# Kernel optimization log

Hardware: AMD Instinct MI355X
Metric: run time of the kernel (lower is better)

## Reference

```python
import jax, jax.numpy as jnp
import numpy as np

D_MODEL = 1024
NUM_HEADS = 16
HEAD_DIM = D_MODEL // NUM_HEADS
THETA = 10000.0


def _trunc_normal(key, shape, std):
    # approximate trunc_normal_(a=-3std, b=3std) by clipping
    return jnp.clip(jax.random.normal(key, shape) * std, -3 * std, 3 * std)


def setup_inputs() -> dict:
    key = jax.random.key(0)
    ks = jax.random.split(key, 6)
    B, S = 2, 2048
    x = jax.random.normal(ks[0], (B, S, D_MODEL), dtype=jnp.float32)
    token_positions = jnp.sort(
        jax.random.randint(ks[1], (B, S), 0, 2048), axis=-1
    ).astype(jnp.int64)
    std = float(np.sqrt(2.0 / (D_MODEL + D_MODEL)))
    Wq = _trunc_normal(ks[2], (D_MODEL, D_MODEL), std)
    Wk = _trunc_normal(ks[3], (D_MODEL, D_MODEL), std)
    Wv = _trunc_normal(ks[4], (D_MODEL, D_MODEL), std)
    Wo = _trunc_normal(ks[5], (D_MODEL, D_MODEL), std)
    return {"x": x, "Wq": Wq, "Wk": Wk, "Wv": Wv, "Wo": Wo,
            "token_positions": token_positions}


def _rope(x, positions):
    # x: (b, h, s, d), positions: (b, s)
    d = x.shape[-1]
    inv_freq = THETA ** (-jnp.arange(0, d, 2, dtype=jnp.float32) / d)  # (d/2,)
    angles = positions.astype(jnp.float32)[:, None, :, None] * inv_freq  # (b,1,s,d/2)
    cos, sin = jnp.cos(angles), jnp.sin(angles)
    x_even, x_odd = x[..., 0::2], x[..., 1::2]
    out_even = x_even * cos - x_odd * sin
    out_odd = x_even * sin + x_odd * cos
    # interleave back: (..., d/2, 2) -> (..., d)
    return jnp.stack([out_even, out_odd], axis=-1).reshape(x.shape)


def reference(x, Wq, Wk, Wv, Wo, token_positions):
    B, S, _ = x.shape
    H, Dh = NUM_HEADS, HEAD_DIM
    # projections: einsum '... i, o i -> ... o'
    q = jnp.einsum('bsi,oi->bso', x, Wq).reshape(B, S, H, Dh).transpose(0, 2, 1, 3)
    k = jnp.einsum('bsi,oi->bso', x, Wk).reshape(B, S, H, Dh).transpose(0, 2, 1, 3)
    v = jnp.einsum('bsi,oi->bso', x, Wv).reshape(B, S, H, Dh).transpose(0, 2, 1, 3)
    q = _rope(q, token_positions)
    k = _rope(k, token_positions)
    scores = jnp.einsum('bhqd,bhkd->bhqk', q.astype(jnp.float32),
                        k.astype(jnp.float32)) / jnp.sqrt(
        jnp.asarray(Dh, dtype=jnp.float32))
    causal = jnp.tril(jnp.ones((S, S), dtype=bool))
    scores = jnp.where(causal, scores, -jnp.inf)
    attn = jax.nn.softmax(scores, axis=-1)
    out = jnp.einsum('bhqk,bhkd->bhqd', attn, v.astype(jnp.float32)).astype(x.dtype)
    out = out.transpose(0, 2, 1, 3).reshape(B, S, H * Dh)
    return jnp.einsum('bsi,oi->bso', out, Wo)
```

## Files before the change

### kernel.cpp

```cpp
#include <hip/hip_runtime.h>
#include <hip/hip_bf16.h>

#define DMODEL 1024
#define NHEADS 16
#define HDIM   64
#define BATCH  2
#define SEQ    2048
#define XELEMS ((size_t)BATCH * SEQ * DMODEL)
#define WELEMS ((size_t)DMODEL * DMODEL)

typedef __attribute__((ext_vector_type(8))) __bf16 bf16x8;
typedef __attribute__((ext_vector_type(4))) float  f32x4;
typedef __attribute__((ext_vector_type(4))) unsigned int   u32x4;
typedef __attribute__((ext_vector_type(4))) unsigned short u16x4;
typedef __attribute__((ext_vector_type(8))) unsigned short u16x8;

typedef const __attribute__((address_space(1))) void* gas_t;
typedef __attribute__((address_space(3))) void* las_t;

static __device__ __forceinline__ unsigned short f2bf(float f) {
  return __builtin_bit_cast(unsigned short, __float2bfloat16(f));
}
static __device__ __forceinline__ float bf2f(unsigned short u) {
  return __bfloat162float(__builtin_bit_cast(__hip_bfloat16, u));
}

__global__ __launch_bounds__(64) void probe_kernel(const unsigned int* __restrict__ x,
                                                   const int* __restrict__ pos,
                                                   int* __restrict__ flags) {
  const int lane = threadIdx.x;
  int bad = 0;
#pragma unroll
  for (int i = 0; i < 32; ++i) {
    const unsigned int u = x[lane * 32 + i];
    if (((u >> 23) & 0xFFu) == 0xFFu) bad++;
  }
  int zodd = 0;
#pragma unroll
  for (int i = 0; i < 4; ++i)
    if (pos[lane * 8 + 2 * i + 1] == 0) zodd++;
#pragma unroll
  for (int s = 1; s < 64; s <<= 1) {
    bad  += __shfl_xor(bad, s);
    zodd += __shfl_xor(zodd, s);
  }
  if (lane == 0) {
    flags[0] = (bad < 64) ? 1 : 0;
    flags[1] = (zodd >= 200) ? 1 : 0;
  }
}

__global__ __launch_bounds__(256) void conv_kernel(
    const void* __restrict__ x,
    const void* __restrict__ w0, const void* __restrict__ w1,
    const void* __restrict__ w2, const void* __restrict__ w3,
    unsigned short* __restrict__ dst, const int* __restrict__ flags) {
  const size_t e = ((size_t)blockIdx.x * 256 + threadIdx.x) * 8;
  const void* src;
  size_t off;
  if (e < XELEMS) { src = x; off = e; }
  else {
    const size_t r = e - XELEMS;
    const int wi = (int)(r >> 20);
    src = (wi == 0) ? w0 : (wi == 1) ? w1 : (wi == 2) ? w2 : w3;
    off = r & (WELEMS - 1);
  }
  if (flags[0]) {
    const float* s = (const float*)src + off;
    const f32x4 a = *(const f32x4*)(s);
    const f32x4 b = *(const f32x4*)(s + 4);
    u16x8 o8;
#pragma unroll
    for (int j = 0; j < 4; ++j) o8[j] = f2bf(a[j]);
#pragma unroll
    for (int j = 0; j < 4; ++j) o8[4 + j] = f2bf(b[j]);
    *(u16x8*)(dst + e) = o8;
  } else {
    *(u32x4*)(dst + e) = *(const u32x4*)((const unsigned short*)src + off);
  }
}

__device__ __forceinline__ void gemm_core(const unsigned short* __restrict__ Ag,
                                          const unsigned short* __restrict__ Bg,
                                          unsigned short* As, unsigned short* Bs,
                                          int bm, int bn, f32x4 acc[4][4]) {
  const int tid = threadIdx.x;
  const int lane = tid & 63;
  const int w  = tid >> 6;
  const int wm = w >> 1, wn = w & 1;
  const int c = lane & 15, g = lane >> 4;
  const int r0 = tid >> 2;
  const int s0 = (tid & 3) * 8;

  auto stage = [&](int buf, int k0) {
    unsigned short* ad = As + buf * 4096;
    unsigned short* bd = Bs + buf * 4096;
    __builtin_amdgcn_global_load_lds((gas_t)(Ag + (size_t)(bm + r0) * DMODEL + k0 + s0),
                                     (las_t)(ad + tid * 8), 16, 0, 0);
    __builtin_amdgcn_global_load_lds((gas_t)(Ag + (size_t)(bm + r0 + 64) * DMODEL + k0 + s0),
                                     (las_t)(ad + (tid + 256) * 8), 16, 0, 0);
    __builtin_amdgcn_global_load_lds((gas_t)(Bg + (size_t)(bn + r0) * DMODEL + k0 + s0),
                                     (las_t)(bd + tid * 8), 16, 0, 0);
    __builtin_amdgcn_global_load_lds((gas_t)(Bg + (size_t)(bn + r0 + 64) * DMODEL + k0 + s0),
                                     (las_t)(bd + (tid + 256) * 8), 16, 0, 0);
  };

  stage(0, 0);
  __syncthreads();
  for (int k0 = 0; k0 < DMODEL; k0 += 32) {
    const int cur = (k0 >> 5) & 1;
    if (k0 + 32 < DMODEL) stage(cur ^ 1, k0 + 32);
    const unsigned short* ar = As + cur * 4096;
    const unsigned short* br = Bs + cur * 4096;
    bf16x8 af[4], bfr[4];
#pragma unroll
    for (int m = 0; m < 4; ++m)
      af[m] = *(const bf16x8*)&ar[(wm * 64 + m * 16 + c) * 32 + g * 8];
#pragma unroll
    for (int n = 0; n < 4; ++n)
      bfr[n] = *(const bf16x8*)&br[(wn * 64 + n * 16 + c) * 32 + g * 8];
#pragma unroll
    for (int m = 0; m < 4; ++m)
#pragma unroll
      for (int n = 0; n < 4; ++n)
        acc[m][n] = __builtin_amdgcn_mfma_f32_16x16x32_bf16(af[m], bfr[n], acc[m][n], 0, 0, 0);
    __syncthreads();
  }
}

__global__ __launch_bounds__(256) void qkv_gemm_kernel(
    const unsigned short* __restrict__ x,
    const unsigned short* __restrict__ Wq, const unsigned short* __restrict__ Wk,
    const unsigned short* __restrict__ Wv,
    unsigned short* __restrict__ qo, unsigned short* __restrict__ ko,
    unsigned short* __restrict__ vto) {
  __shared__ unsigned short As[2 * 128 * 32];
  __shared__ unsigned short Bs[2 * 128 * 32];
  const int z = blockIdx.z;
  const unsigned short* W = (z == 0) ? Wq : (z == 1) ? Wk : Wv;
  const int bm = blockIdx.x * 128, bn = blockIdx.y * 128;
  f32x4 acc[4][4];
#pragma unroll
  for (int m = 0; m < 4; ++m)
#pragma unroll
    for (int n = 0; n < 4; ++n)
#pragma unroll
      for (int j = 0; j < 4; ++j) acc[m][n][j] = 0.f;

  gemm_core(x, W, As, Bs, bm, bn, acc);

  const int tid = threadIdx.x, lane = tid & 63, w = tid >> 6;
  const int wm = w >> 1, wn = w & 1, c = lane & 15, g4 = lane >> 4;
#pragma unroll
  for (int m = 0; m < 4; ++m) {
#pragma unroll
    for (int n = 0; n < 4; ++n) {
      const int col = bn + wn * 64 + n * 16 + c;
      const int h = col >> 6, d = col & 63;
      const int row0 = bm + wm * 64 + m * 16 + g4 * 4;
      if (z == 2) {
        const int b = row0 >> 11, s0 = row0 & (SEQ - 1);
        u16x4 pk;
#pragma unroll
        for (int j = 0; j < 4; ++j) pk[j] = f2bf(acc[m][n][j]);
        *(u16x4*)&vto[((size_t)(b * NHEADS + h) * HDIM + d) * SEQ + s0] = pk;
      } else {
        unsigned short* dst = z ? ko : qo;
#pragma unroll
        for (int j = 0; j < 4; ++j) {
          const int row = row0 + j;
          const int b = row >> 11, s = row & (SEQ - 1);
          dst[((size_t)(b * NHEADS + h) * SEQ + s) * HDIM + d] = f2bf(acc[m][n][j]);
        }
      }
    }
  }
}

__global__ __launch_bounds__(256) void out_gemm_kernel(
    const unsigned short* __restrict__ A, const unsigned short* __restrict__ Wo,
    void* __restrict__ outv, const int* __restrict__ flags) {
  __shared__ unsigned short As[2 * 128 * 32];
  __shared__ unsigned short Bs[2 * 128 * 32];
  const int bm = blockIdx.x * 128, bn = blockIdx.y * 128;
  f32x4 acc[4][4];
#pragma unroll
  for (int m = 0; m < 4; ++m)
#pragma unroll
    for (int n = 0; n < 4; ++n)
#pragma unroll
      for (int j = 0; j < 4; ++j) acc[m][n][j] = 0.f;

  gemm_core(A, Wo, As, Bs, bm, bn, acc);

  const int tid = threadIdx.x, lane = tid & 63, w = tid >> 6;
  const int wm = w >> 1, wn = w & 1, c = lane & 15, g4 = lane >> 4;
  const int f32o = flags[0];
  if (f32o) {
    float* out = (float*)outv;
#pragma unroll
    for (int m = 0; m < 4; ++m)
#pragma unroll
      for (int n = 0; n < 4; ++n) {
        const int col = bn + wn * 64 + n * 16 + c;
#pragma unroll
        for (int j = 0; j < 4; ++j) {
          const int row = bm + wm * 64 + m * 16 + g4 * 4 + j;
          out[(size_t)row * DMODEL + col] = acc[m][n][j];
        }
      }
  } else {
    unsigned short* out = (unsigned short*)outv;
#pragma unroll
    for (int m = 0; m < 4; ++m)
#pragma unroll
      for (int n = 0; n < 4; ++n) {
        const int col = bn + wn * 64 + n * 16 + c;
#pragma unroll
        for (int j = 0; j < 4; ++j) {
          const int row = bm + wm * 64 + m * 16 + g4 * 4 + j;
          out[(size_t)row * DMODEL + col] = f2bf(acc[m][n][j]);
        }
      }
  }
}

__global__ __launch_bounds__(256) void rope_kernel(unsigned short* __restrict__ q,
                                                   unsigned short* __restrict__ k,
                                                   const int* __restrict__ pos,
                                                   const int* __restrict__ flags) {
  const int idx = blockIdx.x * 256 + threadIdx.x;
  const int tsel = idx >> 21;
  const int p = idx & ((1 << 21) - 1);
  const int j = p & 31;
  const int s = (p >> 5) & (SEQ - 1);
  const int bh = p >> 16;
  const int b = bh >> 4;
  unsigned short* base = tsel ? k : q;
  const int pidx = b * SEQ + s;
  const int pv = flags[1] ? pos[2 * pidx] : pos[pidx];
  const float sc = tsel ? 1.0f : 0.125f;
  const float freq = exp2f((float)j * -0.41524101186092026f);
  const float ang = (float)pv * freq;
  const float cs = cosf(ang);
  const float sn = sinf(ang);
  unsigned int* wp = (unsigned int*)base + ((p >> 5) * 32 + j);
  const unsigned int u = *wp;
  const float e = bf2f((unsigned short)(u & 0xffffu));
  const float o = bf2f((unsigned short)(u >> 16));
  *wp = (unsigned int)f2bf((e * cs - o * sn) * sc) |
        ((unsigned int)f2bf((e * sn + o * cs) * sc) << 16);
}

#define MNEG -1e30f
#define QBLK 64
#define LOG2E 1.4426950408889634f
__global__ __launch_bounds__(256, 3) void flash_kernel(
    const unsigned short* __restrict__ q, const unsigned short* __restrict__ k,
    const unsigned short* __restrict__ vt, unsigned short* __restrict__ o) {
  __shared__ unsigned short Ks[2][64 * 64];
  __shared__ unsigned short Vs[2][64 * 64];
  __shared__ unsigned short Ps[64 * 72];

  const int wg = blockIdx.x;
  const int qt = (SEQ / QBLK - 1) - (wg >> 5);
  const int bh = wg & 31;
  const int qbase = qt * QBLK;
  const int tid = threadIdx.x, lane = tid & 63, w = tid >> 6;
  const int c = lane & 15, g = lane >> 4;
  const int wq = w * 16;
  const size_t tb = (size_t)bh * SEQ * HDIM;

  bf16x8 qf[2];
#pragma unroll
  for (int kk = 0; kk < 2; ++kk)
    qf[kk] = *(const bf16x8*)(q + tb + (size_t)(qbase + wq + c) * HDIM + kk * 32 + g * 8);

  auto stageKV = [&](int buf, int kvb) {
#pragma unroll
    for (int i = 0; i < 2; ++i) {
      const int t = tid + i * 256;
      const int r = t >> 3;
      const int sl = (t & 7) ^ (r & 7);
      __builtin_amdgcn_global_load_lds((gas_t)(k + tb + (size_t)(kvb + r) * HDIM + sl * 8),
                                       (las_t)(Ks[buf] + t * 8), 16, 0, 0);
      __builtin_amdgcn_global_load_lds((gas_t)(vt + tb + (size_t)r * SEQ + kvb + sl * 8),
                                       (las_t)(Vs[buf] + t * 8), 16, 0, 0);
    }
  };

  stageKV(0, 0);
  __syncthreads();

  f32x4 acco[4];
#pragma unroll
  for (int n = 0; n < 4; ++n)
#pragma unroll
    for (int j = 0; j < 4; ++j) acco[n][j] = 0.f;
  float m_r = MNEG, l_r = 0.f;

  const int nkv = qt + 1;
  for (int kt = 0; kt < nkv; ++kt) {
    const int p = kt & 1;
    const int kvb = kt * 64;
    if (kt + 1 < nkv) stageKV(p ^ 1, kvb + 64);

    f32x4 accs[4];
#pragma unroll
    for (int n = 0; n < 4; ++n)
#pragma unroll
      for (int j = 0; j < 4; ++j) accs[n][j] = 0.f;
#pragma unroll
    for (int kk = 0; kk < 2; ++kk)
#pragma unroll
      for (int n = 0; n < 4; ++n) {
        const int r = n * 16 + c;
        const int sl = (kk * 4 + g) ^ (r & 7);
        const bf16x8 ak = *(const bf16x8*)&Ks[p][r * 64 + sl * 8];
        accs[n] = __builtin_amdgcn_mfma_f32_16x16x32_bf16(ak, qf[kk], accs[n], 0, 0, 0);
      }

    const int qg = qbase + wq + c;
    if (kt == qt) {
#pragma unroll
      for (int n = 0; n < 4; ++n)
#pragma unroll
        for (int jj = 0; jj < 4; ++jj)
          if (kvb + n * 16 + g * 4 + jj > qg) accs[n][jj] = MNEG;
    }

    float rm = accs[0][0];
#pragma unroll
    for (int n = 0; n < 4; ++n)
#pragma unroll
      for (int jj = 0; jj < 4; ++jj) rm = fmaxf(rm, accs[n][jj]);
    rm = fmaxf(rm, __shfl_xor(rm, 16));
    rm = fmaxf(rm, __shfl_xor(rm, 32));
    if (!__all(rm <= m_r + 8.f)) {
      const float mn = fmaxf(m_r, rm);
      const float al = exp2f((m_r - mn) * LOG2E);
      l_r *= al;
#pragma unroll
      for (int n = 0; n < 4; ++n)
#pragma unroll
        for (int jj = 0; jj < 4; ++jj) acco[n][jj] *= al;
      m_r = mn;
    }
    float rs = 0.f;
#pragma unroll
    for (int n = 0; n < 4; ++n)
#pragma unroll
      for (int jj = 0; jj < 4; ++jj) {
        const float pv = exp2f((accs[n][jj] - m_r) * LOG2E);
        accs[n][jj] = pv;
        rs += pv;
      }
    rs += __shfl_xor(rs, 16);
    rs += __shfl_xor(rs, 32);
    l_r += rs;

#pragma unroll
    for (int n = 0; n < 4; ++n) {
      u16x4 pk4;
#pragma unroll
      for (int jj = 0; jj < 4; ++jj) pk4[jj] = f2bf(accs[n][jj]);
      *(u16x4*)&Ps[(wq + c) * 72 + n * 16 + g * 4] = pk4;
    }

#pragma unroll
    for (int kk = 0; kk < 2; ++kk) {
      const bf16x8 pb = *(const bf16x8*)&Ps[(wq + c) * 72 + kk * 32 + g * 8];
#pragma unroll
      for (int n = 0; n < 4; ++n) {
        const int r = n * 16 + c;
        const int sl = (kk * 4 + g) ^ (r & 7);
        const bf16x8 av = *(const bf16x8*)&Vs[p][r * 64 + sl * 8];
        acco[n] = __builtin_amdgcn_mfma_f32_16x16x32_bf16(av, pb, acco[n], 0, 0, 0);
      }
    }
    __syncthreads();
  }

  const float rl = 1.f / fmaxf(l_r, 1e-20f);
  const int b = bh >> 4, h = bh & 15;
  const int srow = qbase + wq + c;
#pragma unroll
  for (int n = 0; n < 4; ++n) {
    u16x4 pk;
#pragma unroll
    for (int jj = 0; jj < 4; ++jj) pk[jj] = f2bf(acco[n][jj] * rl);
    *(u16x4*)&o[(size_t)(b * SEQ + srow) * DMODEL + h * 64 + n * 16 + g * 4] = pk;
  }
}

extern "C" void kernel_launch(void* const* d_in, const int* in_sizes, int n_in,
                              void* d_out, int out_size, void* d_ws, size_t ws_size,
                              hipStream_t stream) {
  (void)in_sizes; (void)n_in; (void)out_size; (void)ws_size;
  const size_t MB = (size_t)1 << 20;
  char* ws = (char*)d_ws;
  unsigned short* xb  = (unsigned short*)(ws);
  unsigned short* Wqb = (unsigned short*)(ws + 8 * MB);
  unsigned short* Wkb = (unsigned short*)(ws + 10 * MB);
  unsigned short* Wvb = (unsigned short*)(ws + 12 * MB);
  unsigned short* Wob = (unsigned short*)(ws + 14 * MB);
  unsigned short* qw  = (unsigned short*)(ws + 16 * MB);
  unsigned short* kw  = (unsigned short*)(ws + 24 * MB);
  unsigned short* vtw = (unsigned short*)(ws + 32 * MB);
  int* flags          = (int*)(ws + 40 * MB);
  unsigned short* ow  = xb;

  const dim3 blk(256);
  probe_kernel<<<1, 64, 0, stream>>>((const unsigned int*)d_in[0], (const int*)d_in[5], flags);
  conv_kernel<<<4096, blk, 0, stream>>>(d_in[0], d_in[1], d_in[2], d_in[3], d_in[4], xb, flags);
  qkv_gemm_kernel<<<dim3(32, 8, 3), blk, 0, stream>>>(xb, Wqb, Wkb, Wvb, qw, kw, vtw);
  rope_kernel<<<16384, blk, 0, stream>>>(qw, kw, (const int*)d_in[5], flags);
  flash_kernel<<<dim3(1024), blk, 0, stream>>>(qw, kw, vtw, ow);
  out_gemm_kernel<<<dim3(32, 8), blk, 0, stream>>>(ow, Wob, d_out, flags);
}
```

Baseline: 134.5 us.

## Add MFMA setprio, shrink out-proj tile, unroll flash loop with pointer increments

Wraps the MFMA blocks in s_setprio(1)/(0) in the shared GEMM core and the flash kernel, so waves issuing matrix math get scheduling priority. The output projection moves to a 64x128 tile with its own inline mainloop, doubling the grid from 256 to 512 workgroups for better CU occupancy on the small GEMM. The flash attention loop is unrolled by two with compile-time buffer indices and running K/V pointers, which removes per-iteration address arithmetic. Smaller out-proj tiles lower reuse per workgroup and add more loads of Wo.

```diff
diff --git a/kernel.cpp b/kernel.cpp
--- a/kernel.cpp
+++ b/kernel.cpp
@@ -119,11 +119,13 @@
 #pragma unroll
     for (int n = 0; n < 4; ++n)
       bfr[n] = *(const bf16x8*)&br[(wn * 64 + n * 16 + c) * 32 + g * 8];
+    __builtin_amdgcn_s_setprio(1);
 #pragma unroll
     for (int m = 0; m < 4; ++m)
 #pragma unroll
       for (int n = 0; n < 4; ++n)
         acc[m][n] = __builtin_amdgcn_mfma_f32_16x16x32_bf16(af[m], bfr[n], acc[m][n], 0, 0, 0);
+    __builtin_amdgcn_s_setprio(0);
     __syncthreads();
   }
 }
@@ -180,32 +182,65 @@
 __global__ __launch_bounds__(256) void out_gemm_kernel(
     const unsigned short* __restrict__ A, const unsigned short* __restrict__ Wo,
     void* __restrict__ outv, const int* __restrict__ flags) {
-  __shared__ unsigned short As[2 * 128 * 32];
+  __shared__ unsigned short As[2 * 64 * 32];
   __shared__ unsigned short Bs[2 * 128 * 32];
-  const int bm = blockIdx.x * 128, bn = blockIdx.y * 128;
-  f32x4 acc[4][4];
+  const int bm = blockIdx.x * 64, bn = blockIdx.y * 128;
+  const int tid = threadIdx.x, lane = tid & 63, w = tid >> 6;
+  const int c = lane & 15, g = lane >> 4;
+  const int r0 = tid >> 2, s0 = (tid & 3) * 8;
+  f32x4 acc[4][2];
 #pragma unroll
   for (int m = 0; m < 4; ++m)
 #pragma unroll
-    for (int n = 0; n < 4; ++n)
+    for (int n = 0; n < 2; ++n)
 #pragma unroll
       for (int j = 0; j < 4; ++j) acc[m][n][j] = 0.f;
 
-  gemm_core(A, Wo, As, Bs, bm, bn, acc);
-
-  const int tid = threadIdx.x, lane = tid & 63, w = tid >> 6;
-  const int wm = w >> 1, wn = w & 1, c = lane & 15, g4 = lane >> 4;
+  auto stage = [&](int buf, int k0) {
+    __builtin_amdgcn_global_load_lds((gas_t)(A + (size_t)(bm + r0) * DMODEL + k0 + s0),
+                                     (las_t)(As + buf * 2048 + tid * 8), 16, 0, 0);
+    __builtin_amdgcn_global_load_lds((gas_t)(Wo + (size_t)(bn + r0) * DMODEL + k0 + s0),
+                                     (las_t)(Bs + buf * 4096 + tid * 8), 16, 0, 0);
+    __builtin_amdgcn_global_load_lds((gas_t)(Wo + (size_t)(bn + r0 + 64) * DMODEL + k0 + s0),
+                                     (las_t)(Bs + buf * 4096 + (tid + 256) * 8), 16, 0, 0);
+  };
+
+  stage(0, 0);
+  __syncthreads();
+  for (int k0 = 0; k0 < DMODEL; k0 += 32) {
+    const int cur = (k0 >> 5) & 1;
+    if (k0 + 32 < DMODEL) stage(cur ^ 1, k0 + 32);
+    const unsigned short* ar = As + cur * 2048;
+    const unsigned short* br = Bs + cur * 4096;
+    bf16x8 af[4], bfr[2];
+#pragma unroll
+    for (int m = 0; m < 4; ++m)
+      af[m] = *(const bf16x8*)&ar[(m * 16 + c) * 32 + g * 8];
+#pragma unroll
+    for (int n = 0; n < 2; ++n)
+      bfr[n] = *(const bf16x8*)&br[(w * 32 + n * 16 + c) * 32 + g * 8];
+    __builtin_amdgcn_s_setprio(1);
+#pragma unroll
+    for (int m = 0; m < 4; ++m)
+#pragma unroll
+      for (int n = 0; n < 2; ++n)
+        acc[m][n] = __builtin_amdgcn_mfma_f32_16x16x32_bf16(af[m], bfr[n], acc[m][n], 0, 0, 0);
+    __builtin_amdgcn_s_setprio(0);
+    __syncthreads();
+  }
+
+  const int g4 = g;
   const int f32o = flags[0];
   if (f32o) {
     float* out = (float*)outv;
 #pragma unroll
     for (int m = 0; m < 4; ++m)
 #pragma unroll
-      for (int n = 0; n < 4; ++n) {
-        const int col = bn + wn * 64 + n * 16 + c;
+      for (int n = 0; n < 2; ++n) {
+        const int col = bn + w * 32 + n * 16 + c;
 #pragma unroll
         for (int j = 0; j < 4; ++j) {
-          const int row = bm + wm * 64 + m * 16 + g4 * 4 + j;
+          const int row = bm + m * 16 + g4 * 4 + j;
           out[(size_t)row * DMODEL + col] = acc[m][n][j];
         }
       }
@@ -214,11 +249,11 @@
 #pragma unroll
     for (int m = 0; m < 4; ++m)
 #pragma unroll
-      for (int n = 0; n < 4; ++n) {
-        const int col = bn + wn * 64 + n * 16 + c;
+      for (int n = 0; n < 2; ++n) {
+        const int col = bn + w * 32 + n * 16 + c;
 #pragma unroll
         for (int j = 0; j < 4; ++j) {
-          const int row = bm + wm * 64 + m * 16 + g4 * 4 + j;
+          const int row = bm + m * 16 + g4 * 4 + j;
           out[(size_t)row * DMODEL + col] = f2bf(acc[m][n][j]);
         }
       }
@@ -255,6 +290,106 @@
 #define MNEG -1e30f
 #define QBLK 64
 #define LOG2E 1.4426950408889634f
+
+template<int BUF>
+__device__ __forceinline__ void flash_tile(
+    int kt, int nkv, int qt, int qbase, int wq, int c, int g, int tid,
+    const unsigned short* (&kp)[2], const unsigned short* (&vp)[2],
+    unsigned short (&Ks)[2][64 * 64], unsigned short (&Vs)[2][64 * 64],
+    unsigned short (&Ps)[64 * 72],
+    const bf16x8 (&qf)[2], f32x4 (&acco)[4], float& m_r, float& l_r) {
+  const int kvb = kt * 64;
+  if (kt + 1 < nkv) {
+#pragma unroll
+    for (int i = 0; i < 2; ++i) {
+      const int t8 = (tid + i * 256) * 8;
+      __builtin_amdgcn_global_load_lds((gas_t)kp[i], (las_t)(Ks[BUF ^ 1] + t8), 16, 0, 0);
+      __builtin_amdgcn_global_load_lds((gas_t)vp[i], (las_t)(Vs[BUF ^ 1] + t8), 16, 0, 0);
+      kp[i] += 64 * HDIM;
+      vp[i] += 64;
+    }
+  }
+
+  f32x4 accs[4];
+#pragma unroll
+  for (int n = 0; n < 4; ++n)
+#pragma unroll
+    for (int j = 0; j < 4; ++j) accs[n][j] = 0.f;
+  __builtin_amdgcn_s_setprio(1);
+#pragma unroll
+  for (int kk = 0; kk < 2; ++kk)
+#pragma unroll
+    for (int n = 0; n < 4; ++n) {
+      const int r = n * 16 + c;
+      const int sl = (kk * 4 + g) ^ (r & 7);
+      const bf16x8 ak = *(const bf16x8*)&Ks[BUF][r * 64 + sl * 8];
+      accs[n] = __builtin_amdgcn_mfma_f32_16x16x32_bf16(ak, qf[kk], accs[n], 0, 0, 0);
+    }
+  __builtin_amdgcn_s_setprio(0);
+
+  const int qg = qbase + wq + c;
+  if (kt == qt) {
+#pragma unroll
+    for (int n = 0; n < 4; ++n)
+#pragma unroll
+      for (int jj = 0; jj < 4; ++jj)
+        if (kvb + n * 16 + g * 4 + jj > qg) accs[n][jj] = MNEG;
+  }
+
+  float rm = accs[0][0];
+#pragma unroll
+  for (int n = 0; n < 4; ++n)
+#pragma unroll
+    for (int jj = 0; jj < 4; ++jj) rm = fmaxf(rm, accs[n][jj]);
+  rm = fmaxf(rm, __shfl_xor(rm, 16));
+  rm = fmaxf(rm, __shfl_xor(rm, 32));
+  if (!__all(rm <= m_r + 8.f)) {
+    const float mn = fmaxf(m_r, rm);
+    const float al = exp2f((m_r - mn) * LOG2E);
+    l_r *= al;
+#pragma unroll
+    for (int n = 0; n < 4; ++n)
+#pragma unroll
+      for (int jj = 0; jj < 4; ++jj) acco[n][jj] *= al;
+    m_r = mn;
+  }
+  float rs = 0.f;
+#pragma unroll
+  for (int n = 0; n < 4; ++n)
+#pragma unroll
+    for (int jj = 0; jj < 4; ++jj) {
+      const float pv = exp2f((accs[n][jj] - m_r) * LOG2E);
+      accs[n][jj] = pv;
+      rs += pv;
+    }
+  rs += __shfl_xor(rs, 16);
+  rs += __shfl_xor(rs, 32);
+  l_r += rs;
+
+#pragma unroll
+  for (int n = 0; n < 4; ++n) {
+    u16x4 pk4;
+#pragma unroll
+    for (int jj = 0; jj < 4; ++jj) pk4[jj] = f2bf(accs[n][jj]);
+    *(u16x4*)&Ps[(wq + c) * 72 + n * 16 + g * 4] = pk4;
+  }
+
+  __builtin_amdgcn_s_setprio(1);
+#pragma unroll
+  for (int kk = 0; kk < 2; ++kk) {
+    const bf16x8 pb = *(const bf16x8*)&Ps[(wq + c) * 72 + kk * 32 + g * 8];
+#pragma unroll
+    for (int n = 0; n < 4; ++n) {
+      const int r = n * 16 + c;
+      const int sl = (kk * 4 + g) ^ (r & 7);
+      const bf16x8 av = *(const bf16x8*)&Vs[BUF][r * 64 + sl * 8];
+      acco[n] = __builtin_amdgcn_mfma_f32_16x16x32_bf16(av, pb, acco[n], 0, 0, 0);
+    }
+  }
+  __builtin_amdgcn_s_setprio(0);
+  __syncthreads();
+}
+
 __global__ __launch_bounds__(256, 3) void flash_kernel(
     const unsigned short* __restrict__ q, const unsigned short* __restrict__ k,
     const unsigned short* __restrict__ vt, unsigned short* __restrict__ o) {
@@ -276,20 +411,24 @@
   for (int kk = 0; kk < 2; ++kk)
     qf[kk] = *(const bf16x8*)(q + tb + (size_t)(qbase + wq + c) * HDIM + kk * 32 + g * 8);
 
-  auto stageKV = [&](int buf, int kvb) {
-#pragma unroll
-    for (int i = 0; i < 2; ++i) {
-      const int t = tid + i * 256;
-      const int r = t >> 3;
-      const int sl = (t & 7) ^ (r & 7);
-      __builtin_amdgcn_global_load_lds((gas_t)(k + tb + (size_t)(kvb + r) * HDIM + sl * 8),
-                                       (las_t)(Ks[buf] + t * 8), 16, 0, 0);
-      __builtin_amdgcn_global_load_lds((gas_t)(vt + tb + (size_t)r * SEQ + kvb + sl * 8),
-                                       (las_t)(Vs[buf] + t * 8), 16, 0, 0);
-    }
-  };
-
-  stageKV(0, 0);
+  const unsigned short* kp[2];
+  const unsigned short* vp[2];
+#pragma unroll
+  for (int i = 0; i < 2; ++i) {
+    const int t = tid + i * 256;
+    const int r = t >> 3;
+    const int sl = (t & 7) ^ (r & 7);
+    kp[i] = k + tb + (size_t)r * HDIM + sl * 8;
+    vp[i] = vt + tb + (size_t)r * SEQ + sl * 8;
+  }
+#pragma unroll
+  for (int i = 0; i < 2; ++i) {
+    const int t8 = (tid + i * 256) * 8;
+    __builtin_amdgcn_global_load_lds((gas_t)kp[i], (las_t)(Ks[0] + t8), 16, 0, 0);
+    __builtin_amdgcn_global_load_lds((gas_t)vp[i], (las_t)(Vs[0] + t8), 16, 0, 0);
+    kp[i] += 64 * HDIM;
+    vp[i] += 64;
+  }
   __syncthreads();
 
   f32x4 acco[4];
@@ -300,86 +439,13 @@
   float m_r = MNEG, l_r = 0.f;
 
   const int nkv = qt + 1;
-  for (int kt = 0; kt < nkv; ++kt) {
-    const int p = kt & 1;
-    const int kvb = kt * 64;
-    if (kt + 1 < nkv) stageKV(p ^ 1, kvb + 64);
-
-    f32x4 accs[4];
-#pragma unroll
-    for (int n = 0; n < 4; ++n)
-#pragma unroll
-      for (int j = 0; j < 4; ++j) accs[n][j] = 0.f;
-#pragma unroll
-    for (int kk = 0; kk < 2; ++kk)
-#pragma unroll
-      for (int n = 0; n < 4; ++n) {
-        const int r = n * 16 + c;
-        const int sl = (kk * 4 + g) ^ (r & 7);
-        const bf16x8 ak = *(const bf16x8*)&Ks[p][r * 64 + sl * 8];
-        accs[n] = __builtin_amdgcn_mfma_f32_16x16x32_bf16(ak, qf[kk], accs[n], 0, 0, 0);
-      }
-
-    const int qg = qbase + wq + c;
-    if (kt == qt) {
-#pragma unroll
-      for (int n = 0; n < 4; ++n)
-#pragma unroll
-        for (int jj = 0; jj < 4; ++jj)
-          if (kvb + n * 16 + g * 4 + jj > qg) accs[n][jj] = MNEG;
-    }
-
-    float rm = accs[0][0];
-#pragma unroll
-    for (int n = 0; n < 4; ++n)
-#pragma unroll
-      for (int jj = 0; jj < 4; ++jj) rm = fmaxf(rm, accs[n][jj]);
-    rm = fmaxf(rm, __shfl_xor(rm, 16));
-    rm = fmaxf(rm, __shfl_xor(rm, 32));
-    if (!__all(rm <= m_r + 8.f)) {
-      const float mn = fmaxf(m_r, rm);
-      const float al = exp2f((m_r - mn) * LOG2E);
-      l_r *= al;
-#pragma unroll
-      for (int n = 0; n < 4; ++n)
-#pragma unroll
-        for (int jj = 0; jj < 4; ++jj) acco[n][jj] *= al;
-      m_r = mn;
-    }
-    float rs = 0.f;
-#pragma unroll
-    for (int n = 0; n < 4; ++n)
-#pragma unroll
-      for (int jj = 0; jj < 4; ++jj) {
-        const float pv = exp2f((accs[n][jj] - m_r) * LOG2E);
-        accs[n][jj] = pv;
-        rs += pv;
-      }
-    rs += __shfl_xor(rs, 16);
-    rs += __shfl_xor(rs, 32);
-    l_r += rs;
-
-#pragma unroll
-    for (int n = 0; n < 4; ++n) {
-      u16x4 pk4;
-#pragma unroll
-      for (int jj = 0; jj < 4; ++jj) pk4[jj] = f2bf(accs[n][jj]);
-      *(u16x4*)&Ps[(wq + c) * 72 + n * 16 + g * 4] = pk4;
-    }
-
-#pragma unroll
-    for (int kk = 0; kk < 2; ++kk) {
-      const bf16x8 pb = *(const bf16x8*)&Ps[(wq + c) * 72 + kk * 32 + g * 8];
-#pragma unroll
-      for (int n = 0; n < 4; ++n) {
-        const int r = n * 16 + c;
-        const int sl = (kk * 4 + g) ^ (r & 7);
-        const bf16x8 av = *(const bf16x8*)&Vs[p][r * 64 + sl * 8];
-        acco[n] = __builtin_amdgcn_mfma_f32_16x16x32_bf16(av, pb, acco[n], 0, 0, 0);
-      }
-    }
-    __syncthreads();
-  }
+  int kt = 0;
+  for (; kt + 2 <= nkv; kt += 2) {
+    flash_tile<0>(kt,     nkv, qt, qbase, wq, c, g, tid, kp, vp, Ks, Vs, Ps, qf, acco, m_r, l_r);
+    flash_tile<1>(kt + 1, nkv, qt, qbase, wq, c, g, tid, kp, vp, Ks, Vs, Ps, qf, acco, m_r, l_r);
+  }
+  if (kt < nkv)
+    flash_tile<0>(kt, nkv, qt, qbase, wq, c, g, tid, kp, vp, Ks, Vs, Ps, qf, acco, m_r, l_r);
 
   const float rl = 1.f / fmaxf(l_r, 1e-20f);
   const int b = bh >> 4, h = bh & 15;
@@ -416,5 +482,5 @@
   qkv_gemm_kernel<<<dim3(32, 8, 3), blk, 0, stream>>>(xb, Wqb, Wkb, Wvb, qw, kw, vtw);
   rope_kernel<<<16384, blk, 0, stream>>>(qw, kw, (const int*)d_in[5], flags);
   flash_kernel<<<dim3(1024), blk, 0, stream>>>(qw, kw, vtw, ow);
-  out_gemm_kernel<<<dim3(32, 8), blk, 0, stream>>>(ow, Wob, d_out, flags);
-}
+  out_gemm_kernel<<<dim3(64, 8), blk, 0, stream>>>(ow, Wob, d_out, flags);
+}
```

Measured after the change: 122.6 us. 8.8% less time.
